# Performance work log

Measured on AMD Instinct MI355X. Metric: run time of the kernel, lower is better.

## Reference

```python
import jax, jax.numpy as jnp
import numpy as np

N = 8192
D_IN, D_MID, D_EMB = 1024, 256, 64
N_EDGES = N * 8


def setup_inputs() -> dict:
    key = jax.random.key(0)
    ks = jax.random.split(key, 6)
    X = jax.random.normal(ks[0], (N, D_IN), dtype=jnp.float32)
    # Xavier-uniform style init as in get_weight_initial
    b1 = np.sqrt(6.0 / (D_IN + D_MID))
    b2 = np.sqrt(6.0 / (D_MID + D_EMB))
    W1 = jax.random.uniform(ks[1], (D_IN, D_MID), minval=-b1, maxval=b1, dtype=jnp.float32)
    W2 = jax.random.uniform(ks[2], (D_MID, D_EMB), minval=-b2, maxval=b2, dtype=jnp.float32)
    edge_val = jax.random.uniform(ks[3], (N_EDGES,), dtype=jnp.float32)
    edge_src = jax.random.randint(ks[4], (N_EDGES,), 0, N, dtype=jnp.int32)
    edge_dst = jax.random.randint(ks[5], (N_EDGES,), 0, N, dtype=jnp.int32)
    return {"X": X, "W1": W1, "W2": W2, "edge_val": edge_val,
            "edge_src": edge_src, "edge_dst": edge_dst}


def reference(X, W1, W2, edge_val, edge_src, edge_dst):
    n = X.shape[0]

    def spmm(H):  # sparse Laplacian (COO) times dense H
        return jax.ops.segment_sum(edge_val[:, None] * H[edge_src], edge_dst,
                                   num_segments=n)

    h = jax.nn.relu(spmm(X @ W1))          # [N, D_MID]
    emb = spmm(h @ W2)                      # [N, D_EMB]
    # pairwise squared Euclidean distances between rows of emb -> [N, N]
    sq = jnp.sum(emb * emb, axis=1)
    dist = sq[:, None] + sq[None, :] - 2.0 * (emb @ emb.T)
    recons_w = jax.nn.softmax(-dist, axis=1) + 1e-10
    return recons_w
```

## Files before the change

kernel.cpp:

```cpp
#include <hip/hip_runtime.h>
#include <cstddef>

constexpr int NN     = 8192;
constexpr int DIN    = 1024;
constexpr int DMID   = 256;
constexpr int DEMB   = 64;
constexpr int NEDGE  = 65536;
constexpr int MAXDEG = 64;

typedef __attribute__((ext_vector_type(8))) short bf16x8;
typedef __attribute__((ext_vector_type(4))) float f32x4;
#define MFMA16(a, b, c) __builtin_amdgcn_mfma_f32_16x16x32_bf16((a), (b), (c), 0, 0, 0)

__device__ __forceinline__ unsigned short bf16_rne(float x) {
  unsigned u = __float_as_uint(x);
  return (unsigned short)((u + 0x7FFFu + ((u >> 16) & 1u)) >> 16);
}
__device__ __forceinline__ float bf16_tof(unsigned short h) {
  return __uint_as_float((unsigned)h << 16);
}

constexpr int WCONV_BLOCKS = (DMID * DIN + DEMB * DMID) / 256;
constexpr int XCONV_BLOCKS = NN * DIN / (256 * 8);
constexpr int ZERO_BLOCKS  = 16;
__global__ __launch_bounds__(256) void prep_kernel(const float* __restrict__ W1,
                                                   const float* __restrict__ W2,
                                                   const float* __restrict__ X,
                                                   unsigned short* __restrict__ W1b,
                                                   unsigned short* __restrict__ W2b,
                                                   unsigned short* __restrict__ Xb,
                                                   int* __restrict__ zero_base)
{
  int b = blockIdx.x;
  if (b < WCONV_BLOCKS) {
    int idx = b * 256 + threadIdx.x;
    if (idx < DMID * DIN) {
      int n = idx >> 10, k = idx & 1023;
      W1b[idx] = bf16_rne(W1[k * DMID + n]);
    } else {
      int t = idx - DMID * DIN;
      int n = t >> 8, k = t & 255;
      W2b[t] = bf16_rne(W2[k * DEMB + n]);
    }
  } else if (b < WCONV_BLOCKS + XCONV_BLOCKS) {
    int idx = (b - WCONV_BLOCKS) * 2048 + threadIdx.x * 8;
    float4 x0 = *(const float4*)(X + idx);
    float4 x1 = *(const float4*)(X + idx + 4);
    bf16x8 h;
    h[0] = (short)bf16_rne(x0.x); h[1] = (short)bf16_rne(x0.y);
    h[2] = (short)bf16_rne(x0.z); h[3] = (short)bf16_rne(x0.w);
    h[4] = (short)bf16_rne(x1.x); h[5] = (short)bf16_rne(x1.y);
    h[6] = (short)bf16_rne(x1.z); h[7] = (short)bf16_rne(x1.w);
    *(bf16x8*)(Xb + idx) = h;
  } else {
    int idx = (b - WCONV_BLOCKS - XCONV_BLOCKS) * 1024 + threadIdx.x * 4;
    *(int4*)(zero_base + idx) = make_int4(0, 0, 0, 0);
  }
}

__global__ __launch_bounds__(256) void build_ell_kernel(
    const int* __restrict__ esrc, const float* __restrict__ ev,
    const int* __restrict__ edst, int* __restrict__ cursor,
    int* __restrict__ ell_src, float* __restrict__ ell_val)
{
  int e = blockIdx.x * 256 + threadIdx.x;
  int d = edst[e];
  int pos = atomicAdd(&cursor[d], 1);
  if (pos < MAXDEG) {
    ell_src[d * MAXDEG + pos] = esrc[e];
    ell_val[d * MAXDEG + pos] = ev[e];
  }
}

__global__ __launch_bounds__(256) void gemm1_kernel(
    const unsigned short* __restrict__ Xb, const unsigned short* __restrict__ W1b,
    unsigned short* __restrict__ G1)
{
  const int lane = threadIdx.x & 63;
  const int wave = threadIdx.x >> 6;
  const int m0 = blockIdx.x * 64 + wave * 16;
  const int n0 = blockIdx.y * 64;
  const int rl = lane & 15;
  const int kq = (lane >> 4) * 8;
  f32x4 zero = {0.f, 0.f, 0.f, 0.f};
  f32x4 acc[4] = {zero, zero, zero, zero};
  for (int s = 0; s < DIN / 32; ++s) {
    const int kb = s * 32 + kq;
    bf16x8 ah = *(const bf16x8*)(Xb + (size_t)(m0 + rl) * DIN + kb);
#pragma unroll
    for (int ns = 0; ns < 4; ++ns) {
      bf16x8 bh = *(const bf16x8*)(W1b + (size_t)(n0 + ns * 16 + rl) * DIN + kb);
      acc[ns] = MFMA16(ah, bh, acc[ns]);
    }
  }
  const int rq = (lane >> 4) * 4;
#pragma unroll
  for (int ns = 0; ns < 4; ++ns)
#pragma unroll
    for (int r = 0; r < 4; ++r)
      G1[(size_t)(m0 + rq + r) * DMID + n0 + ns * 16 + rl] = bf16_rne(acc[ns][r]);
}

__global__ __launch_bounds__(256) void spmm1_gemm2_kernel(
    const unsigned short* __restrict__ G1, const int* __restrict__ deg,
    const int* __restrict__ ell_src, const float* __restrict__ ell_val,
    const unsigned short* __restrict__ W2b, float* __restrict__ E1)
{
  __shared__ unsigned short Hs[16][DMID + 8];
  const int lane = threadIdx.x & 63;
  const int wave = threadIdx.x >> 6;
  const int r0 = blockIdx.x * 16;
  const int c = lane * 4;
#pragma unroll
  for (int rr = 0; rr < 4; ++rr) {
    const int row = wave * 4 + rr;
    const int r = r0 + row;
    const int dg = min(deg[r], MAXDEG);
    const int* sp = ell_src + (size_t)r * MAXDEG;
    const float* vp = ell_val + (size_t)r * MAXDEG;
    float4 acc = make_float4(0.f, 0.f, 0.f, 0.f);
    for (int e = 0; e < dg; ++e) {
      const int s = sp[e];
      const float v = vp[e];
      ushort4 h = *(const ushort4*)(G1 + (size_t)s * DMID + c);
      acc.x = fmaf(v, bf16_tof(h.x), acc.x);
      acc.y = fmaf(v, bf16_tof(h.y), acc.y);
      acc.z = fmaf(v, bf16_tof(h.z), acc.z);
      acc.w = fmaf(v, bf16_tof(h.w), acc.w);
    }
    ushort4 hq;
    hq.x = bf16_rne(fmaxf(acc.x, 0.f));
    hq.y = bf16_rne(fmaxf(acc.y, 0.f));
    hq.z = bf16_rne(fmaxf(acc.z, 0.f));
    hq.w = bf16_rne(fmaxf(acc.w, 0.f));
    *(ushort4*)(&Hs[row][c]) = hq;
  }
  __syncthreads();
  const int rl = lane & 15;
  const int kq = (lane >> 4) * 8;
  f32x4 acc4 = {0.f, 0.f, 0.f, 0.f};
#pragma unroll
  for (int s = 0; s < DMID / 32; ++s) {
    const int kb = s * 32 + kq;
    bf16x8 a = *(const bf16x8*)(&Hs[rl][kb]);
    bf16x8 b = *(const bf16x8*)(W2b + (size_t)(wave * 16 + rl) * DMID + kb);
    acc4 = MFMA16(a, b, acc4);
  }
  const int rq = (lane >> 4) * 4;
#pragma unroll
  for (int r = 0; r < 4; ++r)
    E1[(size_t)(r0 + rq + r) * DEMB + wave * 16 + rl] = acc4[r];
}

__global__ __launch_bounds__(256) void spmm2_kernel(
    const float* __restrict__ H, const int* __restrict__ deg,
    const int* __restrict__ ell_src, const float* __restrict__ ell_val,
    unsigned short* __restrict__ EmbH, float* __restrict__ sqv)
{
  const int lane = threadIdx.x & 63;
  const int wave = threadIdx.x >> 6;
  const int r = blockIdx.x * 4 + wave;
  const int dg = min(deg[r], MAXDEG);
  const int* sp = ell_src + (size_t)r * MAXDEG;
  const float* vp = ell_val + (size_t)r * MAXDEG;
  float acc = 0.f;
  for (int e = 0; e < dg; ++e)
    acc = fmaf(vp[e], H[(size_t)sp[e] * DEMB + lane], acc);
  unsigned short h = bf16_rne(acc);
  EmbH[(size_t)r * DEMB + lane] = h;
  float hf = bf16_tof(h);
  float sq = hf * hf;
#pragma unroll
  for (int off = 32; off; off >>= 1) sq += __shfl_xor(sq, off, 64);
  if (lane == 0) sqv[r] = sq;
}

__global__ __launch_bounds__(256) void rowsum_kernel(
    const unsigned short* __restrict__ EH, const float* __restrict__ sq,
    float* __restrict__ rowsum)
{
  const int lane = threadIdx.x & 63;
  const int wave = threadIdx.x >> 6;
  const int wr = wave >> 1, wc = wave & 1;
  const int ibase = blockIdx.y * 128 + wr * 64;
  const int rl = lane & 15;
  const int kq = (lane >> 4) * 8;
  const int rq = (lane >> 4) * 4;

  bf16x8 a[2][4];
#pragma unroll
  for (int s = 0; s < 2; ++s)
#pragma unroll
    for (int t = 0; t < 4; ++t)
      a[s][t] = *(const bf16x8*)(EH + (size_t)(ibase + t * 16 + rl) * DEMB + s * 32 + kq);

  float si[4][4];
#pragma unroll
  for (int ms = 0; ms < 4; ++ms)
#pragma unroll
    for (int r = 0; r < 4; ++r) si[ms][r] = sq[ibase + ms * 16 + rq + r];

  float rs[4][4] = {};
  for (int jt = 0; jt < 8; ++jt) {
    const int jbase = blockIdx.x * 1024 + jt * 128 + wc * 64;
    float sj[4];
#pragma unroll
    for (int ns = 0; ns < 4; ++ns) sj[ns] = sq[jbase + ns * 16 + rl];
    f32x4 zero = {0.f, 0.f, 0.f, 0.f};
    f32x4 acc[4][4];
#pragma unroll
    for (int ms = 0; ms < 4; ++ms)
#pragma unroll
      for (int ns = 0; ns < 4; ++ns) acc[ms][ns] = zero;
#pragma unroll
    for (int s = 0; s < 2; ++s) {
      bf16x8 b[4];
#pragma unroll
      for (int t = 0; t < 4; ++t)
        b[t] = *(const bf16x8*)(EH + (size_t)(jbase + t * 16 + rl) * DEMB + s * 32 + kq);
#pragma unroll
      for (int ms = 0; ms < 4; ++ms)
#pragma unroll
        for (int ns = 0; ns < 4; ++ns)
          acc[ms][ns] = MFMA16(a[s][ms], b[ns], acc[ms][ns]);
    }
#pragma unroll
    for (int ms = 0; ms < 4; ++ms)
#pragma unroll
      for (int ns = 0; ns < 4; ++ns)
#pragma unroll
        for (int r = 0; r < 4; ++r)
          rs[ms][r] += __expf(fmaf(2.f, acc[ms][ns][r], -si[ms][r] - sj[ns]));
  }
#pragma unroll
  for (int ms = 0; ms < 4; ++ms)
#pragma unroll
    for (int r = 0; r < 4; ++r) {
      float v = rs[ms][r];
      v += __shfl_xor(v, 1, 64);
      v += __shfl_xor(v, 2, 64);
      v += __shfl_xor(v, 4, 64);
      v += __shfl_xor(v, 8, 64);
      if (rl == 0) atomicAdd(&rowsum[ibase + ms * 16 + rq + r], v);
    }
}

__device__ __forceinline__ void dist_tile_hh(
    const unsigned short* __restrict__ EH, int ibase, int jbase, int lane,
    f32x4 (&acc)[4][4])
{
  const int rl = lane & 15;
  const int kq = (lane >> 4) * 8;
#pragma unroll
  for (int s = 0; s < 2; ++s) {
    const int kb = s * 32 + kq;
    bf16x8 a[4], b[4];
#pragma unroll
    for (int t = 0; t < 4; ++t) {
      a[t] = *(const bf16x8*)(EH + (size_t)(ibase + t * 16 + rl) * DEMB + kb);
      b[t] = *(const bf16x8*)(EH + (size_t)(jbase + t * 16 + rl) * DEMB + kb);
    }
#pragma unroll
    for (int ms = 0; ms < 4; ++ms)
#pragma unroll
      for (int ns = 0; ns < 4; ++ns)
        acc[ms][ns] = MFMA16(a[ms], b[ns], acc[ms][ns]);
  }
}

__global__ __launch_bounds__(256) void dist_write_kernel(
    const unsigned short* __restrict__ EH, const float* __restrict__ sq,
    const float* __restrict__ rowsum, float* __restrict__ out)
{
  const int lane = threadIdx.x & 63;
  const int wave = threadIdx.x >> 6;
  const int wr = wave >> 1, wc = wave & 1;
  const int ibase = blockIdx.y * 128 + wr * 64;
  const int jbase = blockIdx.x * 128 + wc * 64;
  const int rl = lane & 15;
  const int rq = (lane >> 4) * 4;

  f32x4 zero = {0.f, 0.f, 0.f, 0.f};
  f32x4 acc[4][4];
#pragma unroll
  for (int ms = 0; ms < 4; ++ms)
#pragma unroll
    for (int ns = 0; ns < 4; ++ns) acc[ms][ns] = zero;
  dist_tile_hh(EH, ibase, jbase, lane, acc);

  float si[4][4], ri[4][4], sj[4];
#pragma unroll
  for (int ms = 0; ms < 4; ++ms)
#pragma unroll
    for (int r = 0; r < 4; ++r) {
      const int i = ibase + ms * 16 + rq + r;
      si[ms][r] = sq[i];
      ri[ms][r] = 1.f / rowsum[i];
    }
#pragma unroll
  for (int ns = 0; ns < 4; ++ns) sj[ns] = sq[jbase + ns * 16 + rl];

#pragma unroll
  for (int ms = 0; ms < 4; ++ms)
#pragma unroll
    for (int r = 0; r < 4; ++r) {
      const size_t row = (size_t)(ibase + ms * 16 + rq + r) * NN;
#pragma unroll
      for (int ns = 0; ns < 4; ++ns) {
        float e = __expf(fmaf(2.f, acc[ms][ns][r], -si[ms][r] - sj[ns]));
        __builtin_nontemporal_store(fmaf(e, ri[ms][r], 1e-10f),
                                    &out[row + jbase + ns * 16 + rl]);
      }
    }
}

extern "C" void kernel_launch(void* const* d_in, const int* in_sizes, int n_in,
                              void* d_out, int out_size, void* d_ws, size_t ws_size,
                              hipStream_t stream)
{
  const float* X  = (const float*)d_in[0];
  const float* W1 = (const float*)d_in[1];
  const float* W2 = (const float*)d_in[2];
  const float* ev = (const float*)d_in[3];
  const int* esrc = (const int*)d_in[4];
  const int* edst = (const int*)d_in[5];
  float* out = (float*)d_out;

  char* p = (char*)d_ws;
  auto alloc = [&](size_t bytes) { char* q = p; p += (bytes + 255) & ~(size_t)255; return q; };

  int*   cursor  = (int*)alloc(NN * 4);
  float* rowsum  = (float*)alloc(NN * 4);
  float* sqv     = (float*)alloc(NN * 4);
  float* E1      = (float*)alloc((size_t)NN * DEMB * 4);
  unsigned short* W1b  = (unsigned short*)alloc((size_t)DMID * DIN * 2);
  unsigned short* W2b  = (unsigned short*)alloc((size_t)DEMB * DMID * 2);
  unsigned short* Xb   = (unsigned short*)alloc((size_t)NN * DIN * 2);
  unsigned short* G1   = (unsigned short*)alloc((size_t)NN * DMID * 2);
  unsigned short* EmbH = (unsigned short*)alloc((size_t)NN * DEMB * 2);
  int*   ell_src = (int*)alloc((size_t)NN * MAXDEG * 4);
  float* ell_val = (float*)alloc((size_t)NN * MAXDEG * 4);

  prep_kernel<<<WCONV_BLOCKS + XCONV_BLOCKS + ZERO_BLOCKS, 256, 0, stream>>>(
      W1, W2, X, W1b, W2b, Xb, cursor);
  build_ell_kernel<<<NEDGE / 256, 256, 0, stream>>>(esrc, ev, edst, cursor,
                                                    ell_src, ell_val);

  gemm1_kernel<<<dim3(NN / 64, DMID / 64), 256, 0, stream>>>(Xb, W1b, G1);
  spmm1_gemm2_kernel<<<NN / 16, 256, 0, stream>>>(G1, cursor, ell_src, ell_val,
                                                  W2b, E1);
  spmm2_kernel<<<NN / 4, 256, 0, stream>>>(E1, cursor, ell_src, ell_val, EmbH, sqv);

  rowsum_kernel<<<dim3(8, NN / 128), 256, 0, stream>>>(EmbH, sqv, rowsum);
  dist_write_kernel<<<dim3(NN / 128, NN / 128), 256, 0, stream>>>(EmbH, sqv, rowsum, out);
}
```

Before: 434.6 us.

## Fuse all stages into persistent megakernel with software grid barriers

Replaces the seven separate launches (prep, ELL build, GEMM1, SpMM1+GEMM2, SpMM2, rowsum, distance write) with one persistent kernel. Each stage runs as a grid-stride loop, and stages are separated by an atomic-counter grid barrier. The goal is to remove per-launch overhead and the idle gaps between kernels. The SpMM stages also now interleave four rows per wave to expose more memory parallelism. The grid is capped by the occupancy query (at most 512 blocks), so the large output-write stage gets fewer resident blocks to hide latency, and the spin barrier relies on all blocks being co-resident.

```diff
diff --git a/kernel.cpp b/kernel.cpp
--- a/kernel.cpp
+++ b/kernel.cpp
@@ -7,6 +7,7 @@
 constexpr int DEMB   = 64;
 constexpr int NEDGE  = 65536;
 constexpr int MAXDEG = 64;
+constexpr int GRID_MAX = 512;
 
 typedef __attribute__((ext_vector_type(8))) short bf16x8;
 typedef __attribute__((ext_vector_type(4))) float f32x4;
@@ -23,226 +24,19 @@
 constexpr int WCONV_BLOCKS = (DMID * DIN + DEMB * DMID) / 256;
 constexpr int XCONV_BLOCKS = NN * DIN / (256 * 8);
 constexpr int ZERO_BLOCKS  = 16;
-__global__ __launch_bounds__(256) void prep_kernel(const float* __restrict__ W1,
-                                                   const float* __restrict__ W2,
-                                                   const float* __restrict__ X,
-                                                   unsigned short* __restrict__ W1b,
-                                                   unsigned short* __restrict__ W2b,
-                                                   unsigned short* __restrict__ Xb,
-                                                   int* __restrict__ zero_base)
-{
-  int b = blockIdx.x;
-  if (b < WCONV_BLOCKS) {
-    int idx = b * 256 + threadIdx.x;
-    if (idx < DMID * DIN) {
-      int n = idx >> 10, k = idx & 1023;
-      W1b[idx] = bf16_rne(W1[k * DMID + n]);
-    } else {
-      int t = idx - DMID * DIN;
-      int n = t >> 8, k = t & 255;
-      W2b[t] = bf16_rne(W2[k * DEMB + n]);
-    }
-  } else if (b < WCONV_BLOCKS + XCONV_BLOCKS) {
-    int idx = (b - WCONV_BLOCKS) * 2048 + threadIdx.x * 8;
-    float4 x0 = *(const float4*)(X + idx);
-    float4 x1 = *(const float4*)(X + idx + 4);
-    bf16x8 h;
-    h[0] = (short)bf16_rne(x0.x); h[1] = (short)bf16_rne(x0.y);
-    h[2] = (short)bf16_rne(x0.z); h[3] = (short)bf16_rne(x0.w);
-    h[4] = (short)bf16_rne(x1.x); h[5] = (short)bf16_rne(x1.y);
-    h[6] = (short)bf16_rne(x1.z); h[7] = (short)bf16_rne(x1.w);
-    *(bf16x8*)(Xb + idx) = h;
-  } else {
-    int idx = (b - WCONV_BLOCKS - XCONV_BLOCKS) * 1024 + threadIdx.x * 4;
-    *(int4*)(zero_base + idx) = make_int4(0, 0, 0, 0);
-  }
-}
-
-__global__ __launch_bounds__(256) void build_ell_kernel(
-    const int* __restrict__ esrc, const float* __restrict__ ev,
-    const int* __restrict__ edst, int* __restrict__ cursor,
-    int* __restrict__ ell_src, float* __restrict__ ell_val)
-{
-  int e = blockIdx.x * 256 + threadIdx.x;
-  int d = edst[e];
-  int pos = atomicAdd(&cursor[d], 1);
-  if (pos < MAXDEG) {
-    ell_src[d * MAXDEG + pos] = esrc[e];
-    ell_val[d * MAXDEG + pos] = ev[e];
-  }
-}
-
-__global__ __launch_bounds__(256) void gemm1_kernel(
-    const unsigned short* __restrict__ Xb, const unsigned short* __restrict__ W1b,
-    unsigned short* __restrict__ G1)
-{
-  const int lane = threadIdx.x & 63;
-  const int wave = threadIdx.x >> 6;
-  const int m0 = blockIdx.x * 64 + wave * 16;
-  const int n0 = blockIdx.y * 64;
-  const int rl = lane & 15;
-  const int kq = (lane >> 4) * 8;
-  f32x4 zero = {0.f, 0.f, 0.f, 0.f};
-  f32x4 acc[4] = {zero, zero, zero, zero};
-  for (int s = 0; s < DIN / 32; ++s) {
-    const int kb = s * 32 + kq;
-    bf16x8 ah = *(const bf16x8*)(Xb + (size_t)(m0 + rl) * DIN + kb);
-#pragma unroll
-    for (int ns = 0; ns < 4; ++ns) {
-      bf16x8 bh = *(const bf16x8*)(W1b + (size_t)(n0 + ns * 16 + rl) * DIN + kb);
-      acc[ns] = MFMA16(ah, bh, acc[ns]);
-    }
-  }
-  const int rq = (lane >> 4) * 4;
-#pragma unroll
-  for (int ns = 0; ns < 4; ++ns)
-#pragma unroll
-    for (int r = 0; r < 4; ++r)
-      G1[(size_t)(m0 + rq + r) * DMID + n0 + ns * 16 + rl] = bf16_rne(acc[ns][r]);
-}
-
-__global__ __launch_bounds__(256) void spmm1_gemm2_kernel(
-    const unsigned short* __restrict__ G1, const int* __restrict__ deg,
-    const int* __restrict__ ell_src, const float* __restrict__ ell_val,
-    const unsigned short* __restrict__ W2b, float* __restrict__ E1)
-{
-  __shared__ unsigned short Hs[16][DMID + 8];
-  const int lane = threadIdx.x & 63;
-  const int wave = threadIdx.x >> 6;
-  const int r0 = blockIdx.x * 16;
-  const int c = lane * 4;
-#pragma unroll
-  for (int rr = 0; rr < 4; ++rr) {
-    const int row = wave * 4 + rr;
-    const int r = r0 + row;
-    const int dg = min(deg[r], MAXDEG);
-    const int* sp = ell_src + (size_t)r * MAXDEG;
-    const float* vp = ell_val + (size_t)r * MAXDEG;
-    float4 acc = make_float4(0.f, 0.f, 0.f, 0.f);
-    for (int e = 0; e < dg; ++e) {
-      const int s = sp[e];
-      const float v = vp[e];
-      ushort4 h = *(const ushort4*)(G1 + (size_t)s * DMID + c);
-      acc.x = fmaf(v, bf16_tof(h.x), acc.x);
-      acc.y = fmaf(v, bf16_tof(h.y), acc.y);
-      acc.z = fmaf(v, bf16_tof(h.z), acc.z);
-      acc.w = fmaf(v, bf16_tof(h.w), acc.w);
-    }
-    ushort4 hq;
-    hq.x = bf16_rne(fmaxf(acc.x, 0.f));
-    hq.y = bf16_rne(fmaxf(acc.y, 0.f));
-    hq.z = bf16_rne(fmaxf(acc.z, 0.f));
-    hq.w = bf16_rne(fmaxf(acc.w, 0.f));
-    *(ushort4*)(&Hs[row][c]) = hq;
-  }
+
+__device__ __forceinline__ void gsync(int* bar, int phase) {
   __syncthreads();
-  const int rl = lane & 15;
-  const int kq = (lane >> 4) * 8;
-  f32x4 acc4 = {0.f, 0.f, 0.f, 0.f};
-#pragma unroll
-  for (int s = 0; s < DMID / 32; ++s) {
-    const int kb = s * 32 + kq;
-    bf16x8 a = *(const bf16x8*)(&Hs[rl][kb]);
-    bf16x8 b = *(const bf16x8*)(W2b + (size_t)(wave * 16 + rl) * DMID + kb);
-    acc4 = MFMA16(a, b, acc4);
-  }
-  const int rq = (lane >> 4) * 4;
-#pragma unroll
-  for (int r = 0; r < 4; ++r)
-    E1[(size_t)(r0 + rq + r) * DEMB + wave * 16 + rl] = acc4[r];
-}
-
-__global__ __launch_bounds__(256) void spmm2_kernel(
-    const float* __restrict__ H, const int* __restrict__ deg,
-    const int* __restrict__ ell_src, const float* __restrict__ ell_val,
-    unsigned short* __restrict__ EmbH, float* __restrict__ sqv)
-{
-  const int lane = threadIdx.x & 63;
-  const int wave = threadIdx.x >> 6;
-  const int r = blockIdx.x * 4 + wave;
-  const int dg = min(deg[r], MAXDEG);
-  const int* sp = ell_src + (size_t)r * MAXDEG;
-  const float* vp = ell_val + (size_t)r * MAXDEG;
-  float acc = 0.f;
-  for (int e = 0; e < dg; ++e)
-    acc = fmaf(vp[e], H[(size_t)sp[e] * DEMB + lane], acc);
-  unsigned short h = bf16_rne(acc);
-  EmbH[(size_t)r * DEMB + lane] = h;
-  float hf = bf16_tof(h);
-  float sq = hf * hf;
-#pragma unroll
-  for (int off = 32; off; off >>= 1) sq += __shfl_xor(sq, off, 64);
-  if (lane == 0) sqv[r] = sq;
-}
-
-__global__ __launch_bounds__(256) void rowsum_kernel(
-    const unsigned short* __restrict__ EH, const float* __restrict__ sq,
-    float* __restrict__ rowsum)
-{
-  const int lane = threadIdx.x & 63;
-  const int wave = threadIdx.x >> 6;
-  const int wr = wave >> 1, wc = wave & 1;
-  const int ibase = blockIdx.y * 128 + wr * 64;
-  const int rl = lane & 15;
-  const int kq = (lane >> 4) * 8;
-  const int rq = (lane >> 4) * 4;
-
-  bf16x8 a[2][4];
-#pragma unroll
-  for (int s = 0; s < 2; ++s)
-#pragma unroll
-    for (int t = 0; t < 4; ++t)
-      a[s][t] = *(const bf16x8*)(EH + (size_t)(ibase + t * 16 + rl) * DEMB + s * 32 + kq);
-
-  float si[4][4];
-#pragma unroll
-  for (int ms = 0; ms < 4; ++ms)
-#pragma unroll
-    for (int r = 0; r < 4; ++r) si[ms][r] = sq[ibase + ms * 16 + rq + r];
-
-  float rs[4][4] = {};
-  for (int jt = 0; jt < 8; ++jt) {
-    const int jbase = blockIdx.x * 1024 + jt * 128 + wc * 64;
-    float sj[4];
-#pragma unroll
-    for (int ns = 0; ns < 4; ++ns) sj[ns] = sq[jbase + ns * 16 + rl];
-    f32x4 zero = {0.f, 0.f, 0.f, 0.f};
-    f32x4 acc[4][4];
-#pragma unroll
-    for (int ms = 0; ms < 4; ++ms)
-#pragma unroll
-      for (int ns = 0; ns < 4; ++ns) acc[ms][ns] = zero;
-#pragma unroll
-    for (int s = 0; s < 2; ++s) {
-      bf16x8 b[4];
-#pragma unroll
-      for (int t = 0; t < 4; ++t)
-        b[t] = *(const bf16x8*)(EH + (size_t)(jbase + t * 16 + rl) * DEMB + s * 32 + kq);
-#pragma unroll
-      for (int ms = 0; ms < 4; ++ms)
-#pragma unroll
-        for (int ns = 0; ns < 4; ++ns)
-          acc[ms][ns] = MFMA16(a[s][ms], b[ns], acc[ms][ns]);
-    }
-#pragma unroll
-    for (int ms = 0; ms < 4; ++ms)
-#pragma unroll
-      for (int ns = 0; ns < 4; ++ns)
-#pragma unroll
-        for (int r = 0; r < 4; ++r)
-          rs[ms][r] += __expf(fmaf(2.f, acc[ms][ns][r], -si[ms][r] - sj[ns]));
-  }
-#pragma unroll
-  for (int ms = 0; ms < 4; ++ms)
-#pragma unroll
-    for (int r = 0; r < 4; ++r) {
-      float v = rs[ms][r];
-      v += __shfl_xor(v, 1, 64);
-      v += __shfl_xor(v, 2, 64);
-      v += __shfl_xor(v, 4, 64);
-      v += __shfl_xor(v, 8, 64);
-      if (rl == 0) atomicAdd(&rowsum[ibase + ms * 16 + rq + r], v);
-    }
+  if (threadIdx.x == 0) {
+    __threadfence();
+    atomicAdd(bar, 1);
+    const int target = phase * (int)gridDim.x;
+    while (__hip_atomic_load(bar, __ATOMIC_RELAXED, __HIP_MEMORY_SCOPE_AGENT)
+           < target)
+      __builtin_amdgcn_s_sleep(2);
+    __threadfence();
+  }
+  __syncthreads();
 }
 
 __device__ __forceinline__ void dist_tile_hh(
@@ -268,50 +62,287 @@
   }
 }
 
-__global__ __launch_bounds__(256) void dist_write_kernel(
-    const unsigned short* __restrict__ EH, const float* __restrict__ sq,
-    const float* __restrict__ rowsum, float* __restrict__ out)
+__global__ __launch_bounds__(256, 2) void mega_kernel(
+    const float* __restrict__ X, const float* __restrict__ W1,
+    const float* __restrict__ W2, const float* __restrict__ ev,
+    const int* __restrict__ esrc, const int* __restrict__ edst,
+    float* __restrict__ out,
+    int* __restrict__ cursor, float* __restrict__ rowsum,
+    float* __restrict__ sqv, float* __restrict__ E1,
+    unsigned short* __restrict__ W1b, unsigned short* __restrict__ W2b,
+    unsigned short* __restrict__ Xb, unsigned short* __restrict__ G1,
+    unsigned short* __restrict__ EmbH,
+    int* __restrict__ ell_src, float* __restrict__ ell_val,
+    int* bar)
 {
   const int lane = threadIdx.x & 63;
   const int wave = threadIdx.x >> 6;
-  const int wr = wave >> 1, wc = wave & 1;
-  const int ibase = blockIdx.y * 128 + wr * 64;
-  const int jbase = blockIdx.x * 128 + wc * 64;
-  const int rl = lane & 15;
-  const int rq = (lane >> 4) * 4;
-
-  f32x4 zero = {0.f, 0.f, 0.f, 0.f};
-  f32x4 acc[4][4];
-#pragma unroll
-  for (int ms = 0; ms < 4; ++ms)
-#pragma unroll
-    for (int ns = 0; ns < 4; ++ns) acc[ms][ns] = zero;
-  dist_tile_hh(EH, ibase, jbase, lane, acc);
-
-  float si[4][4], ri[4][4], sj[4];
-#pragma unroll
-  for (int ms = 0; ms < 4; ++ms)
-#pragma unroll
-    for (int r = 0; r < 4; ++r) {
-      const int i = ibase + ms * 16 + rq + r;
-      si[ms][r] = sq[i];
-      ri[ms][r] = 1.f / rowsum[i];
-    }
-#pragma unroll
-  for (int ns = 0; ns < 4; ++ns) sj[ns] = sq[jbase + ns * 16 + rl];
-
-#pragma unroll
-  for (int ms = 0; ms < 4; ++ms)
-#pragma unroll
-    for (int r = 0; r < 4; ++r) {
-      const size_t row = (size_t)(ibase + ms * 16 + rq + r) * NN;
+
+  for (int b = blockIdx.x; b < WCONV_BLOCKS + XCONV_BLOCKS + ZERO_BLOCKS;
+       b += gridDim.x) {
+    if (b < WCONV_BLOCKS) {
+      int idx = b * 256 + threadIdx.x;
+      if (idx < DMID * DIN) {
+        int n = idx >> 10, k = idx & 1023;
+        W1b[idx] = bf16_rne(W1[k * DMID + n]);
+      } else {
+        int t = idx - DMID * DIN;
+        int n = t >> 8, k = t & 255;
+        W2b[t] = bf16_rne(W2[k * DEMB + n]);
+      }
+    } else if (b < WCONV_BLOCKS + XCONV_BLOCKS) {
+      int idx = (b - WCONV_BLOCKS) * 2048 + threadIdx.x * 8;
+      float4 x0 = *(const float4*)(X + idx);
+      float4 x1 = *(const float4*)(X + idx + 4);
+      bf16x8 h;
+      h[0] = (short)bf16_rne(x0.x); h[1] = (short)bf16_rne(x0.y);
+      h[2] = (short)bf16_rne(x0.z); h[3] = (short)bf16_rne(x0.w);
+      h[4] = (short)bf16_rne(x1.x); h[5] = (short)bf16_rne(x1.y);
+      h[6] = (short)bf16_rne(x1.z); h[7] = (short)bf16_rne(x1.w);
+      *(bf16x8*)(Xb + idx) = h;
+    } else {
+      int idx = (b - WCONV_BLOCKS - XCONV_BLOCKS) * 1024 + threadIdx.x * 4;
+      *(int4*)(cursor + idx) = make_int4(0, 0, 0, 0);
+    }
+  }
+  gsync(bar, 1);
+
+  for (int b = blockIdx.x; b < NEDGE / 256; b += gridDim.x) {
+    int e = b * 256 + threadIdx.x;
+    int d = edst[e];
+    int pos = atomicAdd(&cursor[d], 1);
+    if (pos < MAXDEG) {
+      ell_src[d * MAXDEG + pos] = esrc[e];
+      ell_val[d * MAXDEG + pos] = ev[e];
+    }
+  }
+  gsync(bar, 2);
+
+  for (int vb = blockIdx.x; vb < (NN / 64) * (DMID / 64); vb += gridDim.x) {
+    const int m0 = (vb & 127) * 64 + wave * 16;
+    const int n0 = (vb >> 7) * 64;
+    const int rl = lane & 15;
+    const int kq = (lane >> 4) * 8;
+    f32x4 zero = {0.f, 0.f, 0.f, 0.f};
+    f32x4 acc[4] = {zero, zero, zero, zero};
+    for (int s = 0; s < DIN / 32; ++s) {
+      const int kb = s * 32 + kq;
+      bf16x8 ah = *(const bf16x8*)(Xb + (size_t)(m0 + rl) * DIN + kb);
 #pragma unroll
       for (int ns = 0; ns < 4; ++ns) {
-        float e = __expf(fmaf(2.f, acc[ms][ns][r], -si[ms][r] - sj[ns]));
-        __builtin_nontemporal_store(fmaf(e, ri[ms][r], 1e-10f),
-                                    &out[row + jbase + ns * 16 + rl]);
-      }
-    }
+        bf16x8 bh = *(const bf16x8*)(W1b + (size_t)(n0 + ns * 16 + rl) * DIN + kb);
+        acc[ns] = MFMA16(ah, bh, acc[ns]);
+      }
+    }
+    const int rq = (lane >> 4) * 4;
+#pragma unroll
+    for (int ns = 0; ns < 4; ++ns)
+#pragma unroll
+      for (int r = 0; r < 4; ++r)
+        G1[(size_t)(m0 + rq + r) * DMID + n0 + ns * 16 + rl] = bf16_rne(acc[ns][r]);
+  }
+  gsync(bar, 3);
+
+  {
+    __shared__ unsigned short Hs[16][DMID + 8];
+    for (int vb = blockIdx.x; vb < NN / 16; vb += gridDim.x) {
+      const int rbase = vb * 16 + wave * 4;
+      int dg[4]; const int* sp[4]; const float* vp[4];
+      int dgm = 0;
+#pragma unroll
+      for (int rr = 0; rr < 4; ++rr) {
+        dg[rr] = min(cursor[rbase + rr], MAXDEG);
+        dgm = max(dgm, dg[rr]);
+        sp[rr] = ell_src + (size_t)(rbase + rr) * MAXDEG;
+        vp[rr] = ell_val + (size_t)(rbase + rr) * MAXDEG;
+      }
+      const int c = lane * 4;
+      float4 acc[4];
+#pragma unroll
+      for (int rr = 0; rr < 4; ++rr) acc[rr] = make_float4(0.f, 0.f, 0.f, 0.f);
+      for (int e = 0; e < dgm; ++e) {
+#pragma unroll
+        for (int rr = 0; rr < 4; ++rr) {
+          if (e < dg[rr]) {
+            const int s   = sp[rr][e];
+            const float v = vp[rr][e];
+            ushort4 h = *(const ushort4*)(G1 + (size_t)s * DMID + c);
+            acc[rr].x = fmaf(v, bf16_tof(h.x), acc[rr].x);
+            acc[rr].y = fmaf(v, bf16_tof(h.y), acc[rr].y);
+            acc[rr].z = fmaf(v, bf16_tof(h.z), acc[rr].z);
+            acc[rr].w = fmaf(v, bf16_tof(h.w), acc[rr].w);
+          }
+        }
+      }
+#pragma unroll
+      for (int rr = 0; rr < 4; ++rr) {
+        ushort4 hq;
+        hq.x = bf16_rne(fmaxf(acc[rr].x, 0.f));
+        hq.y = bf16_rne(fmaxf(acc[rr].y, 0.f));
+        hq.z = bf16_rne(fmaxf(acc[rr].z, 0.f));
+        hq.w = bf16_rne(fmaxf(acc[rr].w, 0.f));
+        *(ushort4*)(&Hs[wave * 4 + rr][c]) = hq;
+      }
+      __syncthreads();
+      const int rl = lane & 15;
+      const int kq = (lane >> 4) * 8;
+      f32x4 acc4 = {0.f, 0.f, 0.f, 0.f};
+#pragma unroll
+      for (int s = 0; s < DMID / 32; ++s) {
+        const int kb = s * 32 + kq;
+        bf16x8 a = *(const bf16x8*)(&Hs[rl][kb]);
+        bf16x8 b = *(const bf16x8*)(W2b + (size_t)(wave * 16 + rl) * DMID + kb);
+        acc4 = MFMA16(a, b, acc4);
+      }
+      const int rq = (lane >> 4) * 4;
+#pragma unroll
+      for (int r = 0; r < 4; ++r)
+        E1[(size_t)(vb * 16 + rq + r) * DEMB + wave * 16 + rl] = acc4[r];
+      __syncthreads();
+    }
+  }
+  gsync(bar, 4);
+
+  for (int vb = blockIdx.x; vb < NN / 16; vb += gridDim.x) {
+    const int rbase = vb * 16 + wave * 4;
+    int dg[4]; const int* sp[4]; const float* vp[4];
+    int dgm = 0;
+#pragma unroll
+    for (int rr = 0; rr < 4; ++rr) {
+      dg[rr] = min(cursor[rbase + rr], MAXDEG);
+      dgm = max(dgm, dg[rr]);
+      sp[rr] = ell_src + (size_t)(rbase + rr) * MAXDEG;
+      vp[rr] = ell_val + (size_t)(rbase + rr) * MAXDEG;
+    }
+    float acc[4] = {0.f, 0.f, 0.f, 0.f};
+    for (int e = 0; e < dgm; ++e) {
+#pragma unroll
+      for (int rr = 0; rr < 4; ++rr)
+        if (e < dg[rr])
+          acc[rr] = fmaf(vp[rr][e], E1[(size_t)sp[rr][e] * DEMB + lane], acc[rr]);
+    }
+#pragma unroll
+    for (int rr = 0; rr < 4; ++rr) {
+      unsigned short h = bf16_rne(acc[rr]);
+      EmbH[(size_t)(rbase + rr) * DEMB + lane] = h;
+      float hf = bf16_tof(h);
+      float sq = hf * hf;
+#pragma unroll
+      for (int off = 32; off; off >>= 1) sq += __shfl_xor(sq, off, 64);
+      if (lane == 0) sqv[rbase + rr] = sq;
+    }
+  }
+  gsync(bar, 5);
+
+  for (int vb = blockIdx.x; vb < 8 * (NN / 128); vb += gridDim.x) {
+    const int by = vb >> 3, bx = vb & 7;
+    const int wr = wave >> 1, wc = wave & 1;
+    const int ibase = by * 128 + wr * 64;
+    const int rl = lane & 15;
+    const int kq = (lane >> 4) * 8;
+    const int rq = (lane >> 4) * 4;
+
+    bf16x8 a[2][4];
+#pragma unroll
+    for (int s = 0; s < 2; ++s)
+#pragma unroll
+      for (int t = 0; t < 4; ++t)
+        a[s][t] = *(const bf16x8*)(EmbH + (size_t)(ibase + t * 16 + rl) * DEMB
+                                   + s * 32 + kq);
+    float si[4][4];
+#pragma unroll
+    for (int ms = 0; ms < 4; ++ms)
+#pragma unroll
+      for (int r = 0; r < 4; ++r) si[ms][r] = sqv[ibase + ms * 16 + rq + r];
+
+    float rs[4][4] = {};
+    for (int jt = 0; jt < 8; ++jt) {
+      const int jbase = bx * 1024 + jt * 128 + wc * 64;
+      float sj[4];
+#pragma unroll
+      for (int ns = 0; ns < 4; ++ns) sj[ns] = sqv[jbase + ns * 16 + rl];
+      f32x4 zero = {0.f, 0.f, 0.f, 0.f};
+      f32x4 acc[4][4];
+#pragma unroll
+      for (int ms = 0; ms < 4; ++ms)
+#pragma unroll
+        for (int ns = 0; ns < 4; ++ns) acc[ms][ns] = zero;
+#pragma unroll
+      for (int s = 0; s < 2; ++s) {
+        bf16x8 b[4];
+#pragma unroll
+        for (int t = 0; t < 4; ++t)
+          b[t] = *(const bf16x8*)(EmbH + (size_t)(jbase + t * 16 + rl) * DEMB
+                                  + s * 32 + kq);
+#pragma unroll
+        for (int ms = 0; ms < 4; ++ms)
+#pragma unroll
+          for (int ns = 0; ns < 4; ++ns)
+            acc[ms][ns] = MFMA16(a[s][ms], b[ns], acc[ms][ns]);
+      }
+#pragma unroll
+      for (int ms = 0; ms < 4; ++ms)
+#pragma unroll
+        for (int ns = 0; ns < 4; ++ns)
+#pragma unroll
+          for (int r = 0; r < 4; ++r)
+            rs[ms][r] += __expf(fmaf(2.f, acc[ms][ns][r], -si[ms][r] - sj[ns]));
+    }
+#pragma unroll
+    for (int ms = 0; ms < 4; ++ms)
+#pragma unroll
+      for (int r = 0; r < 4; ++r) {
+        float v = rs[ms][r];
+        v += __shfl_xor(v, 1, 64);
+        v += __shfl_xor(v, 2, 64);
+        v += __shfl_xor(v, 4, 64);
+        v += __shfl_xor(v, 8, 64);
+        if (rl == 0) atomicAdd(&rowsum[ibase + ms * 16 + rq + r], v);
+      }
+  }
+  gsync(bar, 6);
+
+  for (int vb = blockIdx.x; vb < (NN / 128) * (NN / 128); vb += gridDim.x) {
+    const int bi = vb >> 6, bj = vb & 63;
+    const int wr = wave >> 1, wc = wave & 1;
+    const int ibase = bi * 128 + wr * 64;
+    const int jbase = bj * 128 + wc * 64;
+    const int rl = lane & 15;
+    const int rq = (lane >> 4) * 4;
+
+    f32x4 zero = {0.f, 0.f, 0.f, 0.f};
+    f32x4 acc[4][4];
+#pragma unroll
+    for (int ms = 0; ms < 4; ++ms)
+#pragma unroll
+      for (int ns = 0; ns < 4; ++ns) acc[ms][ns] = zero;
+    dist_tile_hh(EmbH, ibase, jbase, lane, acc);
+
+    float si[4][4], ri[4][4], sj[4];
+#pragma unroll
+    for (int ms = 0; ms < 4; ++ms)
+#pragma unroll
+      for (int r = 0; r < 4; ++r) {
+        const int i = ibase + ms * 16 + rq + r;
+        si[ms][r] = sqv[i];
+        ri[ms][r] = 1.f / rowsum[i];
+      }
+#pragma unroll
+    for (int ns = 0; ns < 4; ++ns) sj[ns] = sqv[jbase + ns * 16 + rl];
+
+#pragma unroll
+    for (int ms = 0; ms < 4; ++ms)
+#pragma unroll
+      for (int r = 0; r < 4; ++r) {
+        const size_t row = (size_t)(ibase + ms * 16 + rq + r) * NN;
+#pragma unroll
+        for (int ns = 0; ns < 4; ++ns) {
+          float e = __expf(fmaf(2.f, acc[ms][ns][r], -si[ms][r] - sj[ns]));
+          __builtin_nontemporal_store(fmaf(e, ri[ms][r], 1e-10f),
+                                      &out[row + jbase + ns * 16 + rl]);
+        }
+      }
+  }
 }
 
 extern "C" void kernel_launch(void* const* d_in, const int* in_sizes, int n_in,
@@ -329,6 +360,7 @@
   char* p = (char*)d_ws;
   auto alloc = [&](size_t bytes) { char* q = p; p += (bytes + 255) & ~(size_t)255; return q; };
 
+  int*   bar     = (int*)alloc(256);
   int*   cursor  = (int*)alloc(NN * 4);
   float* rowsum  = (float*)alloc(NN * 4);
   float* sqv     = (float*)alloc(NN * 4);
@@ -341,16 +373,16 @@
   int*   ell_src = (int*)alloc((size_t)NN * MAXDEG * 4);
   float* ell_val = (float*)alloc((size_t)NN * MAXDEG * 4);
 
-  prep_kernel<<<WCONV_BLOCKS + XCONV_BLOCKS + ZERO_BLOCKS, 256, 0, stream>>>(
-      W1, W2, X, W1b, W2b, Xb, cursor);
-  build_ell_kernel<<<NEDGE / 256, 256, 0, stream>>>(esrc, ev, edst, cursor,
-                                                    ell_src, ell_val);
-
-  gemm1_kernel<<<dim3(NN / 64, DMID / 64), 256, 0, stream>>>(Xb, W1b, G1);
-  spmm1_gemm2_kernel<<<NN / 16, 256, 0, stream>>>(G1, cursor, ell_src, ell_val,
-                                                  W2b, E1);
-  spmm2_kernel<<<NN / 4, 256, 0, stream>>>(E1, cursor, ell_src, ell_val, EmbH, sqv);
-
-  rowsum_kernel<<<dim3(8, NN / 128), 256, 0, stream>>>(EmbH, sqv, rowsum);
-  dist_write_kernel<<<dim3(NN / 128, NN / 128), 256, 0, stream>>>(EmbH, sqv, rowsum, out);
-}
+  int occ = 0;
+  if (hipOccupancyMaxActiveBlocksPerMultiprocessor(&occ, mega_kernel, 256, 0)
+      != hipSuccess || occ < 1)
+    occ = 1;
+  int grid = occ * 256;
+  if (grid > GRID_MAX) grid = GRID_MAX;
+
+  hipMemsetAsync(bar, 0, 4, stream);
+  mega_kernel<<<grid, 256, 0, stream>>>(X, W1, W2, ev, esrc, edst, out,
+                                        cursor, rowsum, sqv, E1,
+                                        W1b, W2b, Xb, G1, EmbH,
+                                        ell_src, ell_val, bar);
+}
```

Result: slower. 606.5 us (+39.6%).

## Shrink distance tiles to 128x64, add more rowsum blocks, use exp2 with prescaled norms

Applied to the files above, without the earlier changes.

Halves the column width of each wave's distance tile (64x32 instead of 64x64) in both the rowsum and the output-writing kernels. This doubles the grid sizes and adds occupancy hints through launch_bounds(256,4). Squared norms are premultiplied by log2(e) so the exponent becomes a single exp2 with a fused 2*log2(e) coefficient. Rowsum no longer keeps A fragments resident in registers and reloads them every tile, trading extra global loads for fewer registers and more waves in flight.

```diff
diff --git a/kernel.cpp b/kernel.cpp
--- a/kernel.cpp
+++ b/kernel.cpp
@@ -11,6 +11,9 @@
 typedef __attribute__((ext_vector_type(8))) short bf16x8;
 typedef __attribute__((ext_vector_type(4))) float f32x4;
 #define MFMA16(a, b, c) __builtin_amdgcn_mfma_f32_16x16x32_bf16((a), (b), (c), 0, 0, 0)
+
+constexpr float LOG2E    = 1.44269504088896340736f;
+constexpr float TWOLOG2E = 2.88539008177792681472f;
 
 __device__ __forceinline__ unsigned short bf16_rne(float x) {
   unsigned u = __float_as_uint(x);
@@ -172,10 +175,34 @@
   float sq = hf * hf;
 #pragma unroll
   for (int off = 32; off; off >>= 1) sq += __shfl_xor(sq, off, 64);
-  if (lane == 0) sqv[r] = sq;
-}
-
-__global__ __launch_bounds__(256) void rowsum_kernel(
+  if (lane == 0) sqv[r] = sq * LOG2E;
+}
+
+__device__ __forceinline__ void dist_tile_32(
+    const unsigned short* __restrict__ EH, int ibase, int jbase, int lane,
+    f32x4 (&acc)[4][2])
+{
+  const int rl = lane & 15;
+  const int kq = (lane >> 4) * 8;
+#pragma unroll
+  for (int s = 0; s < 2; ++s) {
+    const int kb = s * 32 + kq;
+    bf16x8 a[4], b[2];
+#pragma unroll
+    for (int t = 0; t < 4; ++t)
+      a[t] = *(const bf16x8*)(EH + (size_t)(ibase + t * 16 + rl) * DEMB + kb);
+#pragma unroll
+    for (int t = 0; t < 2; ++t)
+      b[t] = *(const bf16x8*)(EH + (size_t)(jbase + t * 16 + rl) * DEMB + kb);
+#pragma unroll
+    for (int ms = 0; ms < 4; ++ms)
+#pragma unroll
+      for (int ns = 0; ns < 2; ++ns)
+        acc[ms][ns] = MFMA16(a[ms], b[ns], acc[ms][ns]);
+  }
+}
+
+__global__ __launch_bounds__(256, 4) void rowsum_kernel(
     const unsigned short* __restrict__ EH, const float* __restrict__ sq,
     float* __restrict__ rowsum)
 {
@@ -184,15 +211,7 @@
   const int wr = wave >> 1, wc = wave & 1;
   const int ibase = blockIdx.y * 128 + wr * 64;
   const int rl = lane & 15;
-  const int kq = (lane >> 4) * 8;
   const int rq = (lane >> 4) * 4;
-
-  bf16x8 a[2][4];
-#pragma unroll
-  for (int s = 0; s < 2; ++s)
-#pragma unroll
-    for (int t = 0; t < 4; ++t)
-      a[s][t] = *(const bf16x8*)(EH + (size_t)(ibase + t * 16 + rl) * DEMB + s * 32 + kq);
 
   float si[4][4];
 #pragma unroll
@@ -202,35 +221,25 @@
 
   float rs[4][4] = {};
   for (int jt = 0; jt < 8; ++jt) {
-    const int jbase = blockIdx.x * 1024 + jt * 128 + wc * 64;
-    float sj[4];
-#pragma unroll
-    for (int ns = 0; ns < 4; ++ns) sj[ns] = sq[jbase + ns * 16 + rl];
+    const int jbase = blockIdx.x * 512 + jt * 64 + wc * 32;
+    float sj[2];
+#pragma unroll
+    for (int ns = 0; ns < 2; ++ns) sj[ns] = sq[jbase + ns * 16 + rl];
     f32x4 zero = {0.f, 0.f, 0.f, 0.f};
-    f32x4 acc[4][4];
+    f32x4 acc[4][2];
 #pragma unroll
     for (int ms = 0; ms < 4; ++ms)
 #pragma unroll
-      for (int ns = 0; ns < 4; ++ns) acc[ms][ns] = zero;
-#pragma unroll
-    for (int s = 0; s < 2; ++s) {
-      bf16x8 b[4];
-#pragma unroll
-      for (int t = 0; t < 4; ++t)
-        b[t] = *(const bf16x8*)(EH + (size_t)(jbase + t * 16 + rl) * DEMB + s * 32 + kq);
-#pragma unroll
-      for (int ms = 0; ms < 4; ++ms)
-#pragma unroll
-        for (int ns = 0; ns < 4; ++ns)
-          acc[ms][ns] = MFMA16(a[s][ms], b[ns], acc[ms][ns]);
-    }
+      for (int ns = 0; ns < 2; ++ns) acc[ms][ns] = zero;
+    dist_tile_32(EH, ibase, jbase, lane, acc);
 #pragma unroll
     for (int ms = 0; ms < 4; ++ms)
 #pragma unroll
-      for (int ns = 0; ns < 4; ++ns)
+      for (int ns = 0; ns < 2; ++ns)
 #pragma unroll
         for (int r = 0; r < 4; ++r)
-          rs[ms][r] += __expf(fmaf(2.f, acc[ms][ns][r], -si[ms][r] - sj[ns]));
+          rs[ms][r] += __builtin_exp2f(
+              fmaf(TWOLOG2E, acc[ms][ns][r], -si[ms][r] - sj[ns]));
   }
 #pragma unroll
   for (int ms = 0; ms < 4; ++ms)
@@ -245,30 +254,7 @@
     }
 }
 
-__device__ __forceinline__ void dist_tile_hh(
-    const unsigned short* __restrict__ EH, int ibase, int jbase, int lane,
-    f32x4 (&acc)[4][4])
-{
-  const int rl = lane & 15;
-  const int kq = (lane >> 4) * 8;
-#pragma unroll
-  for (int s = 0; s < 2; ++s) {
-    const int kb = s * 32 + kq;
-    bf16x8 a[4], b[4];
-#pragma unroll
-    for (int t = 0; t < 4; ++t) {
-      a[t] = *(const bf16x8*)(EH + (size_t)(ibase + t * 16 + rl) * DEMB + kb);
-      b[t] = *(const bf16x8*)(EH + (size_t)(jbase + t * 16 + rl) * DEMB + kb);
-    }
-#pragma unroll
-    for (int ms = 0; ms < 4; ++ms)
-#pragma unroll
-      for (int ns = 0; ns < 4; ++ns)
-        acc[ms][ns] = MFMA16(a[ms], b[ns], acc[ms][ns]);
-  }
-}
-
-__global__ __launch_bounds__(256) void dist_write_kernel(
+__global__ __launch_bounds__(256, 4) void dist_write_kernel(
     const unsigned short* __restrict__ EH, const float* __restrict__ sq,
     const float* __restrict__ rowsum, float* __restrict__ out)
 {
@@ -276,19 +262,19 @@
   const int wave = threadIdx.x >> 6;
   const int wr = wave >> 1, wc = wave & 1;
   const int ibase = blockIdx.y * 128 + wr * 64;
-  const int jbase = blockIdx.x * 128 + wc * 64;
+  const int jbase = blockIdx.x * 64 + wc * 32;
   const int rl = lane & 15;
   const int rq = (lane >> 4) * 4;
 
   f32x4 zero = {0.f, 0.f, 0.f, 0.f};
-  f32x4 acc[4][4];
-#pragma unroll
-  for (int ms = 0; ms < 4; ++ms)
-#pragma unroll
-    for (int ns = 0; ns < 4; ++ns) acc[ms][ns] = zero;
-  dist_tile_hh(EH, ibase, jbase, lane, acc);
-
-  float si[4][4], ri[4][4], sj[4];
+  f32x4 acc[4][2];
+#pragma unroll
+  for (int ms = 0; ms < 4; ++ms)
+#pragma unroll
+    for (int ns = 0; ns < 2; ++ns) acc[ms][ns] = zero;
+  dist_tile_32(EH, ibase, jbase, lane, acc);
+
+  float si[4][4], ri[4][4], sj[2];
 #pragma unroll
   for (int ms = 0; ms < 4; ++ms)
 #pragma unroll
@@ -298,7 +284,7 @@
       ri[ms][r] = 1.f / rowsum[i];
     }
 #pragma unroll
-  for (int ns = 0; ns < 4; ++ns) sj[ns] = sq[jbase + ns * 16 + rl];
+  for (int ns = 0; ns < 2; ++ns) sj[ns] = sq[jbase + ns * 16 + rl];
 
 #pragma unroll
   for (int ms = 0; ms < 4; ++ms)
@@ -306,8 +292,9 @@
     for (int r = 0; r < 4; ++r) {
       const size_t row = (size_t)(ibase + ms * 16 + rq + r) * NN;
 #pragma unroll
-      for (int ns = 0; ns < 4; ++ns) {
-        float e = __expf(fmaf(2.f, acc[ms][ns][r], -si[ms][r] - sj[ns]));
+      for (int ns = 0; ns < 2; ++ns) {
+        float e = __builtin_exp2f(
+            fmaf(TWOLOG2E, acc[ms][ns][r], -si[ms][r] - sj[ns]));
         __builtin_nontemporal_store(fmaf(e, ri[ms][r], 1e-10f),
                                     &out[row + jbase + ns * 16 + rl]);
       }
@@ -351,6 +338,7 @@
                                                   W2b, E1);
   spmm2_kernel<<<NN / 4, 256, 0, stream>>>(E1, cursor, ell_src, ell_val, EmbH, sqv);
 
-  rowsum_kernel<<<dim3(8, NN / 128), 256, 0, stream>>>(EmbH, sqv, rowsum);
-  dist_write_kernel<<<dim3(NN / 128, NN / 128), 256, 0, stream>>>(EmbH, sqv, rowsum, out);
-}
+  rowsum_kernel<<<dim3(NN / 512, NN / 128), 256, 0, stream>>>(EmbH, sqv, rowsum);
+  dist_write_kernel<<<dim3(NN / 64, NN / 128), 256, 0, stream>>>(EmbH, sqv, rowsum,
+                                                                 out);
+}
```

New measurement: 439.5 us. Within noise of the previous version (+1.1%).
